# Performance work log

Measured on AMD Instinct MI355X. Metric: run time of the kernel, lower is better.

Reference implementation:

```python
import jax, jax.numpy as jnp
import numpy as np

N_NODES = 100000
N_EDGES = 300000
N_GRAPHS = 128
NODE_VOCAB = 200
NODE_DIM = 128
EDGE_VOCAB = 8
EDGE_DIM = 64
K_LAYERS = 3


def setup_inputs() -> dict:
    key = jax.random.key(0)
    ks = iter(jax.random.split(key, 40))
    f = lambda shape: jax.random.normal(next(ks), shape, dtype=jnp.float32)
    s = lambda shape: f(shape) * 0.05
    inp = {}
    inp["x_s"] = f((N_NODES, NODE_VOCAB))
    inp["x_t"] = f((N_NODES, NODE_VOCAB))
    inp["edge_attr_s"] = f((2 * N_EDGES, EDGE_VOCAB))
    inp["edge_attr_t"] = f((2 * N_EDGES, EDGE_VOCAB))
    inp["edge_index_s"] = jax.random.randint(next(ks), (2, N_EDGES), 0, N_NODES)
    inp["edge_index_t"] = jax.random.randint(next(ks), (2, N_EDGES), 0, N_NODES)
    inp["x_s_batch"] = jnp.sort(jax.random.randint(next(ks), (N_NODES,), 0, N_GRAPHS))
    inp["x_t_batch"] = jnp.sort(jax.random.randint(next(ks), (N_NODES,), 0, N_GRAPHS))
    inp["y"] = jax.random.randint(next(ks), (N_GRAPHS,), 0, 2)
    cat = 2 * NODE_DIM + EDGE_DIM  # 320: [x_src, edge_attr, x_dst]
    inp["node_emb"] = s((NODE_VOCAB, NODE_DIM))
    inp["edge_emb"] = s((EDGE_VOCAB, EDGE_DIM))
    inp["W_in_0"] = s((K_LAYERS, cat, EDGE_DIM))
    inp["W_in_1"] = s((K_LAYERS, EDGE_DIM, 1))
    inp["W_out_0"] = s((K_LAYERS, cat, EDGE_DIM))
    inp["W_out_1"] = s((K_LAYERS, EDGE_DIM, 1))
    inp["Wg_in"] = s((K_LAYERS, NODE_DIM, NODE_DIM))
    inp["bg_in"] = jnp.zeros((K_LAYERS, NODE_DIM), jnp.float32)
    inp["Wg_out"] = s((K_LAYERS, NODE_DIM, NODE_DIM))
    inp["bg_out"] = jnp.zeros((K_LAYERS, NODE_DIM), jnp.float32)
    inp["cls_W0"] = s((2 * NODE_DIM, NODE_DIM))
    inp["cls_b0"] = jnp.zeros((NODE_DIM,), jnp.float32)
    inp["cls_W1"] = s((NODE_DIM, 2))
    inp["cls_b1"] = jnp.zeros((2,), jnp.float32)
    return inp


def _dag_embed(x, e, row, col, W_in_0, W_in_1, W_out_0, W_out_1, Wg_in, bg_in, Wg_out, bg_out):
    N = x.shape[0]
    E = row.shape[0]
    for k in range(W_in_0.shape[0]):
        e_in, e_out = e[:E], e[E:]  # chunk(edge_attr_x, 2, dim=0)
        info_in = jnp.concatenate([x[row], e_in, x[col]], axis=1)   # [E, 2D+Ce]
        info_out = jnp.concatenate([x[col], e_out, x[row]], axis=1)
        e_in = info_in @ W_in_0[k]
        e_out = info_out @ W_out_0[k]
        w_in = jax.nn.sigmoid(e_in @ W_in_1[k]).ravel()   # [E]
        w_out = jax.nn.sigmoid(e_out @ W_out_1[k]).ravel()
        # embedding_in: flow source->target (x_j = x[row], aggregate at col)
        xi = x @ Wg_in[k]
        x_in = jax.ops.segment_sum(w_in[:, None] * xi[row], col, num_segments=N) + bg_in[k]
        # embedding_out: flow target->source (x_j = x[col], aggregate at row)
        xo = x @ Wg_out[k]
        x_out = jax.ops.segment_sum(w_out[:, None] * xo[col], row, num_segments=N) + bg_out[k]
        x = x + x_in + x_out
        e = jnp.concatenate([e_in, e_out], axis=0)
    return x


def _mean_pool(x, batch, num_graphs):
    sums = jax.ops.segment_sum(x, batch, num_segments=num_graphs)
    cnt = jax.ops.segment_sum(jnp.ones((x.shape[0], 1), x.dtype), batch, num_segments=num_graphs)
    return sums / jnp.maximum(cnt, 1.0)


def reference(x_s, x_t, edge_attr_s, edge_attr_t, edge_index_s, edge_index_t,
              x_s_batch, x_t_batch, y, node_emb, edge_emb,
              W_in_0, W_in_1, W_out_0, W_out_1, Wg_in, bg_in, Wg_out, bg_out,
              cls_W0, cls_b0, cls_W1, cls_b1):
    # Initialization: argmax -> embedding lookup
    h_s = node_emb[jnp.argmax(x_s, axis=1)]
    h_t = node_emb[jnp.argmax(x_t, axis=1)]
    he_s = edge_emb[jnp.argmax(edge_attr_s, axis=1)]
    he_t = edge_emb[jnp.argmax(edge_attr_t, axis=1)]
    h_s = _dag_embed(h_s, he_s, edge_index_s[0], edge_index_s[1],
                     W_in_0, W_in_1, W_out_0, W_out_1, Wg_in, bg_in, Wg_out, bg_out)
    h_t = _dag_embed(h_t, he_t, edge_index_t[0], edge_index_t[1],
                     W_in_0, W_in_1, W_out_0, W_out_1, Wg_in, bg_in, Wg_out, bg_out)
    g_s = _mean_pool(h_s, x_s_batch, N_GRAPHS)
    g_t = _mean_pool(h_t, x_t_batch, N_GRAPHS)
    h = jax.nn.relu(jnp.concatenate([g_s, g_t], axis=1) @ cls_W0 + cls_b0)
    logits = h @ cls_W1 + cls_b1
    logp = jax.nn.log_softmax(logits, axis=1)
    loss = -jnp.mean(jnp.take_along_axis(logp, y[:, None], axis=1))
    return loss
```

## Files before the change

### kernel.cpp

```cpp
#include <hip/hip_runtime.h>
#include <hip/hip_bf16.h>

#define N_NODES 100000
#define N_EDGES 300000
#define N_GRAPHS 128
#define NODE_VOCAB 200
#define NODE_DIM 128
#define EDGE_DIM 64
#define K_LAYERS 3

#define SCAN_CHUNK 2048
#define SCAN_NBLK ((N_NODES + SCAN_CHUNK - 1) / SCAN_CHUNK)

typedef unsigned short ushort_t;
typedef __attribute__((ext_vector_type(8))) __bf16 bf16x8;
typedef __attribute__((ext_vector_type(4))) float f32x4;

__device__ inline ushort_t f2bf(float f) {
    unsigned int u = __float_as_uint(f);
    unsigned int r = (u + 0x7fff + ((u >> 16) & 1)) >> 16;
    return (ushort_t)r;
}
__device__ inline float bf2f(ushort_t u) {
    return __uint_as_float(((unsigned int)u) << 16);
}
__device__ inline float bflo(unsigned int u) { return __uint_as_float(u << 16); }
__device__ inline float bfhi(unsigned int u) { return __uint_as_float(u & 0xffff0000u); }

#define MASK_J0 0x15151515u
#define MASK_J1 0x28282828u
#define MASK_J2 0x40404040u

__device__ ushort_t g_hb[2][(size_t)N_NODES * NODE_DIM];
__device__ ushort_t g_XWx_b[(size_t)N_NODES * 256];
__device__ ushort_t g_WcatT[256 * 128];
__device__ ushort_t g_QT[K_LAYERS][32][128];
__device__ float g_scal[(size_t)N_NODES * 32];
__device__ float g_bias[8][6];
__device__ int  g_evoc[2 * N_EDGES];
__device__ float g_gsum[2][N_GRAPHS * NODE_DIM];
__device__ float g_cnt[2][N_GRAPHS];
__device__ float g_H[N_GRAPHS * NODE_DIM];
__device__ int  g_deg_in[N_NODES];
__device__ int  g_deg_out[N_NODES];
__device__ int  g_off_in[N_NODES + 1];
__device__ int  g_off_out[N_NODES + 1];
__device__ int  g_cur_in[N_NODES];
__device__ int  g_cur_out[N_NODES];
__device__ int2 g_lst_in[N_EDGES];
__device__ int2 g_lst_out[N_EDGES];
__device__ int  g_bsum[2][SCAN_NBLK];
__device__ int  g_boff[2][SCAN_NBLK];

__global__ void node_embed_kernel(const float* __restrict__ x, const float* __restrict__ emb,
                                  int N) {
    int wave = threadIdx.x >> 6;
    int lane = threadIdx.x & 63;
    int n = blockIdx.x * 4 + wave;
    if (n >= N) return;
    const float* xr = x + (size_t)n * NODE_VOCAB;
    float v = xr[lane];
    int idx = lane;
    float nv = xr[lane + 64];
    if (nv > v) { v = nv; idx = lane + 64; }
    nv = xr[lane + 128];
    if (nv > v) { v = nv; idx = lane + 128; }
    if (lane < NODE_VOCAB - 192) {
        nv = xr[lane + 192];
        if (nv > v) { v = nv; idx = lane + 192; }
    }
    #pragma unroll
    for (int off = 32; off; off >>= 1) {
        float ov = __shfl_xor(v, off);
        int oi = __shfl_xor(idx, off);
        if (ov > v || (ov == v && oi < idx)) { v = ov; idx = oi; }
    }
    const float* er = emb + (size_t)idx * NODE_DIM;
    g_hb[0][(size_t)n * NODE_DIM + lane] = f2bf(er[lane]);
    g_hb[0][(size_t)n * NODE_DIM + 64 + lane] = f2bf(er[64 + lane]);
}

__global__ void edge_voc_kernel(const float* __restrict__ ea, int M) {
    long idx = (long)blockIdx.x * 256 + threadIdx.x;
    if (idx >= M) return;
    const float* ar = ea + idx * 8;
    float4 v0 = *(const float4*)ar;
    float4 v1 = *(const float4*)(ar + 4);
    float vals[8] = {v0.x, v0.y, v0.z, v0.w, v1.x, v1.y, v1.z, v1.w};
    int best = 0;
    float bv = vals[0];
    #pragma unroll
    for (int i = 1; i < 8; ++i)
        if (vals[i] > bv) { bv = vals[i]; best = i; }
    g_evoc[idx] = best;
}

__global__ void zero_qt_kernel() {
    int i = blockIdx.x * 256 + threadIdx.x;
    if (i < K_LAYERS * 32 * 128) ((ushort_t*)g_QT)[i] = 0;
}

__global__ void setup_gates_kernel(const float* __restrict__ Wi0, const float* __restrict__ Wi1,
                                   const float* __restrict__ Wo0, const float* __restrict__ Wo1,
                                   const float* __restrict__ eemb) {
    int b = blockIdx.x;
    int D = b / 3, k = b % 3;
    int t = threadIdx.x;
    const float* W0 = D ? Wo0 : Wi0;
    const float* W1 = D ? Wo1 : Wi1;
    __shared__ float u[64], un[64];
    if (t < 64) u[t] = W1[k * 64 + t];
    __syncthreads();
    int offk = (k == 0) ? 0 : (k == 1 ? 2 : 4);
    for (int j = k; j >= 0; --j) {
        const float* Wj = W0 + (size_t)j * 320 * 64;
        float qa = 0.f, qc = 0.f;
        for (int m = 0; m < 64; ++m) {
            float um = u[m];
            qa += Wj[t * 64 + m] * um;
            qc += Wj[(192 + t) * 64 + m] * um;
        }
        g_QT[j][(D ? 8 : 0) + offk + j][t] = f2bf(qa);
        g_QT[j][(D ? 24 : 16) + offk + j][t] = f2bf(qc);
        float s = 0.f;
        if (t < 64) {
            for (int m = 0; m < 64; ++m) s += Wj[(128 + t) * 64 + m] * u[m];
        }
        __syncthreads();
        if (t < 64) un[t] = s;
        __syncthreads();
        if (t < 64) u[t] = un[t];
        __syncthreads();
    }
    if (t < 8) {
        float s = 0.f;
        for (int m = 0; m < 64; ++m) s += eemb[t * 64 + m] * u[m];
        g_bias[t][D * 3 + k] = s;
    }
}

__global__ void csr_zero_kernel() {
    int i = blockIdx.x * 256 + threadIdx.x;
    if (i < N_NODES) { g_deg_in[i] = 0; g_deg_out[i] = 0; }
}

__global__ void csr_count_kernel(const int* __restrict__ row, const int* __restrict__ col,
                                 int E) {
    int e = blockIdx.x * 256 + threadIdx.x;
    if (e >= E) return;
    atomicAdd(&g_deg_in[col[e]], 1);
    atomicAdd(&g_deg_out[row[e]], 1);
}

__global__ void csr_bsum_kernel() {
    int which = blockIdx.y;
    const int* deg = which ? g_deg_out : g_deg_in;
    int b = blockIdx.x;
    int t = threadIdx.x;
    int base = b * SCAN_CHUNK;
    int s = 0;
    #pragma unroll
    for (int i = 0; i < SCAN_CHUNK / 256; ++i) {
        int idx = base + i * 256 + t;
        if (idx < N_NODES) s += deg[idx];
    }
    __shared__ int red[256];
    red[t] = s;
    __syncthreads();
    for (int d = 128; d; d >>= 1) {
        if (t < d) red[t] += red[t + d];
        __syncthreads();
    }
    if (t == 0) g_bsum[which][b] = red[0];
}

__global__ void csr_bscan_kernel() {
    int which = blockIdx.x;
    int t = threadIdx.x;
    int v = (t < SCAN_NBLK) ? g_bsum[which][t] : 0;
    int orig = v;
    #pragma unroll
    for (int d = 1; d < 64; d <<= 1) {
        int u = __shfl_up(v, d, 64);
        if (t >= d) v += u;
    }
    if (t < SCAN_NBLK) g_boff[which][t] = v - orig;
}

__global__ void csr_off_kernel(int total) {
    int which = blockIdx.y;
    const int* deg = which ? g_deg_out : g_deg_in;
    int* off = which ? g_off_out : g_off_in;
    int* cur = which ? g_cur_out : g_cur_in;
    int b = blockIdx.x;
    int t = threadIdx.x;
    const int per = SCAN_CHUNK / 256;
    int lo = b * SCAN_CHUNK + t * per;
    int d8[per];
    int s = 0;
    #pragma unroll
    for (int i = 0; i < per; ++i) {
        int idx = lo + i;
        d8[i] = (idx < N_NODES) ? deg[idx] : 0;
        s += d8[i];
    }
    __shared__ int part[256];
    part[t] = s;
    __syncthreads();
    for (int d = 1; d < 256; d <<= 1) {
        int add = (t >= d) ? part[t - d] : 0;
        __syncthreads();
        part[t] += add;
        __syncthreads();
    }
    int run = g_boff[which][b] + part[t] - s;
    #pragma unroll
    for (int i = 0; i < per; ++i) {
        int idx = lo + i;
        if (idx < N_NODES) {
            off[idx] = run;
            cur[idx] = run;
            run += d8[i];
        }
    }
    if (b == 0 && t == 0) off[N_NODES] = total;
}

__global__ void csr_fill_kernel(const int* __restrict__ row, const int* __restrict__ col,
                                int E) {
    int e = blockIdx.x * 256 + threadIdx.x;
    if (e >= E) return;
    int r = row[e], c = col[e];
    int p = atomicAdd(&g_cur_in[c], 1);
    g_lst_in[p] = make_int2(r, g_evoc[e]);
    int q = atomicAdd(&g_cur_out[r], 1);
    g_lst_out[q] = make_int2(c, g_evoc[E + e]);
}

__global__ void assemble_wcat(const float* __restrict__ Wgi, const float* __restrict__ Wgo) {
    int idx = blockIdx.x * 256 + threadIdx.x;
    int n = idx >> 7;
    int kd = idx & 127;
    float v = (n < 128) ? Wgi[kd * 128 + n] : Wgo[kd * 128 + (n - 128)];
    g_WcatT[n * 128 + kd] = f2bf(v);
}

__global__ __launch_bounds__(320) void gemm_xw_mfma(int cur, int layer, unsigned int mask,
                                                    int M) {
    const ushort_t* __restrict__ hb = g_hb[cur];
    int m0 = blockIdx.x * 64;
    int t = threadIdx.x;
    int wave = t >> 6, lane = t & 63;
    __shared__ ushort_t As[64 * 128];

    for (int idx = t; idx < 1024; idx += 320) {
        int m = idx >> 4, c = idx & 15;
        int gm = m0 + m;
        uint4 v = make_uint4(0u, 0u, 0u, 0u);
        if (gm < M) v = *(const uint4*)(hb + (size_t)gm * 128 + c * 8);
        *(uint4*)&As[m * 128 + ((c * 8) ^ ((m & 7) << 3))] = v;
    }
    __syncthreads();

    int lr = lane & 15, lk = lane >> 4;

    if (wave < 4) {
        int nbase = wave * 64;
        f32x4 acc[4][4];
        #pragma unroll
        for (int i = 0; i < 4; ++i)
            #pragma unroll
            for (int j = 0; j < 4; ++j)
                acc[i][j] = (f32x4){0.f, 0.f, 0.f, 0.f};

        const ushort_t* Bbase = g_WcatT + (size_t)nbase * 128;
        #pragma unroll
        for (int ks = 0; ks < 4; ++ks) {
            bf16x8 a[4], b[4];
            int ke = ks * 32 + lk * 8;
            #pragma unroll
            for (int mt = 0; mt < 4; ++mt) {
                int row = mt * 16 + lr;
                a[mt] = *(const bf16x8*)&As[row * 128 + (ke ^ ((row & 7) << 3))];
            }
            #pragma unroll
            for (int nt = 0; nt < 4; ++nt) {
                b[nt] = *(const bf16x8*)(Bbase + (size_t)(nt * 16 + lr) * 128 + ke);
            }
            #pragma unroll
            for (int mt = 0; mt < 4; ++mt)
                #pragma unroll
                for (int nt = 0; nt < 4; ++nt)
                    acc[mt][nt] = __builtin_amdgcn_mfma_f32_16x16x32_bf16(a[mt], b[nt], acc[mt][nt], 0, 0, 0);
        }

        #pragma unroll
        for (int mt = 0; mt < 4; ++mt) {
            #pragma unroll
            for (int r = 0; r < 4; ++r) {
                int gm = m0 + mt * 16 + lk * 4 + r;
                if (gm >= M) continue;
                #pragma unroll
                for (int nt = 0; nt < 4; ++nt) {
                    int n = nbase + nt * 16 + lr;
                    g_XWx_b[(size_t)gm * 256 + n] = f2bf(acc[mt][nt][r]);
                }
            }
        }
    } else {
        const ushort_t* QT = &g_QT[layer][0][0];
        f32x4 acc[4][2];
        #pragma unroll
        for (int i = 0; i < 4; ++i)
            #pragma unroll
            for (int j = 0; j < 2; ++j)
                acc[i][j] = (f32x4){0.f, 0.f, 0.f, 0.f};

        #pragma unroll
        for (int ks = 0; ks < 4; ++ks) {
            bf16x8 a[4], b[2];
            int ke = ks * 32 + lk * 8;
            #pragma unroll
            for (int mt = 0; mt < 4; ++mt) {
                int row = mt * 16 + lr;
                a[mt] = *(const bf16x8*)&As[row * 128 + (ke ^ ((row & 7) << 3))];
            }
            #pragma unroll
            for (int nt = 0; nt < 2; ++nt)
                b[nt] = *(const bf16x8*)&QT[(nt * 16 + lr) * 128 + ke];
            #pragma unroll
            for (int mt = 0; mt < 4; ++mt)
                #pragma unroll
                for (int nt = 0; nt < 2; ++nt)
                    acc[mt][nt] = __builtin_amdgcn_mfma_f32_16x16x32_bf16(a[mt], b[nt], acc[mt][nt], 0, 0, 0);
        }

        #pragma unroll
        for (int mt = 0; mt < 4; ++mt)
            #pragma unroll
            for (int r = 0; r < 4; ++r) {
                int gm = m0 + mt * 16 + lk * 4 + r;
                if (gm >= M) continue;
                #pragma unroll
                for (int nt = 0; nt < 2; ++nt) {
                    int colc = nt * 16 + lr;
                    if ((mask >> colc) & 1u)
                        g_scal[(size_t)gm * 32 + colc] = acc[mt][nt][r];
                }
            }
    }
}

__global__ __launch_bounds__(256) void aggregate_kernel(int cur, int k,
                                                        const float* __restrict__ bgi,
                                                        const float* __restrict__ bgo, int N) {
    int wv = threadIdx.x >> 6;
    int lane = threadIdx.x & 63;
    int grp = lane >> 4, li = lane & 15;
    int n = blockIdx.x * 4 + wv;
    if (n >= N) return;
    float bias_in = g_bias[lane & 7][k];
    float bias_out = g_bias[lane & 7][3 + k];
    const float* srow = g_scal + (size_t)n * 32;
    float cin, cout;
    if (k == 0) {
        cin = srow[16]; cout = srow[24];
    } else if (k == 1) {
        float2 a = *(const float2*)(srow + 18);
        float2 b = *(const float2*)(srow + 26);
        cin = a.x + a.y; cout = b.x + b.y;
    } else {
        float4 a = *(const float4*)(srow + 20);
        float4 b = *(const float4*)(srow + 28);
        cin = a.x + a.y + a.z; cout = b.x + b.y + b.z;
    }
    float acc[8];
    if (grp == 0) {
        uint4 xv = *(const uint4*)(g_hb[cur] + (size_t)n * 128 + li * 8);
        float4 b1 = *(const float4*)(bgi + li * 8);
        float4 b2 = *(const float4*)(bgi + li * 8 + 4);
        float4 c1 = *(const float4*)(bgo + li * 8);
        float4 c2 = *(const float4*)(bgo + li * 8 + 4);
        acc[0] = bflo(xv.x) + b1.x + c1.x;
        acc[1] = bfhi(xv.x) + b1.y + c1.y;
        acc[2] = bflo(xv.y) + b1.z + c1.z;
        acc[3] = bfhi(xv.y) + b1.w + c1.w;
        acc[4] = bflo(xv.z) + b2.x + c2.x;
        acc[5] = bfhi(xv.z) + b2.y + c2.y;
        acc[6] = bflo(xv.w) + b2.z + c2.z;
        acc[7] = bfhi(xv.w) + b2.w + c2.w;
    } else {
        #pragma unroll
        for (int q = 0; q < 8; ++q) acc[q] = 0.f;
    }
    int p0 = g_off_in[n], p1 = g_off_in[n + 1];
    for (int p = p0 + grp; p < p1; p += 4) {
        int2 se = g_lst_in[p];
        const float* arow = g_scal + (size_t)se.x * 32;
        float asum;
        if (k == 0) asum = arow[0];
        else if (k == 1) { float2 t2 = *(const float2*)(arow + 2); asum = t2.x + t2.y; }
        else { float4 t4 = *(const float4*)(arow + 4); asum = t4.x + t4.y + t4.z; }
        float s = __shfl(bias_in, se.y) + asum + cin;
        float wvv = 1.0f / (1.0f + __expf(-s));
        uint4 pv = *(const uint4*)(g_XWx_b + (size_t)se.x * 256 + li * 8);
        acc[0] += wvv * bflo(pv.x);
        acc[1] += wvv * bfhi(pv.x);
        acc[2] += wvv * bflo(pv.y);
        acc[3] += wvv * bfhi(pv.y);
        acc[4] += wvv * bflo(pv.z);
        acc[5] += wvv * bfhi(pv.z);
        acc[6] += wvv * bflo(pv.w);
        acc[7] += wvv * bfhi(pv.w);
    }
    p0 = g_off_out[n]; p1 = g_off_out[n + 1];
    for (int p = p0 + grp; p < p1; p += 4) {
        int2 se = g_lst_out[p];
        const float* arow = g_scal + (size_t)se.x * 32;
        float asum;
        if (k == 0) asum = arow[8];
        else if (k == 1) { float2 t2 = *(const float2*)(arow + 10); asum = t2.x + t2.y; }
        else { float4 t4 = *(const float4*)(arow + 12); asum = t4.x + t4.y + t4.z; }
        float s = __shfl(bias_out, se.y) + asum + cout;
        float wvv = 1.0f / (1.0f + __expf(-s));
        uint4 pv = *(const uint4*)(g_XWx_b + (size_t)se.x * 256 + 128 + li * 8);
        acc[0] += wvv * bflo(pv.x);
        acc[1] += wvv * bfhi(pv.x);
        acc[2] += wvv * bflo(pv.y);
        acc[3] += wvv * bfhi(pv.y);
        acc[4] += wvv * bflo(pv.z);
        acc[5] += wvv * bfhi(pv.z);
        acc[6] += wvv * bflo(pv.w);
        acc[7] += wvv * bfhi(pv.w);
    }
    #pragma unroll
    for (int q = 0; q < 8; ++q) {
        acc[q] += __shfl_xor(acc[q], 16);
        acc[q] += __shfl_xor(acc[q], 32);
    }
    if (grp == 0) {
        uint4 pk;
        pk.x = ((unsigned int)f2bf(acc[1]) << 16) | (unsigned int)f2bf(acc[0]);
        pk.y = ((unsigned int)f2bf(acc[3]) << 16) | (unsigned int)f2bf(acc[2]);
        pk.z = ((unsigned int)f2bf(acc[5]) << 16) | (unsigned int)f2bf(acc[4]);
        pk.w = ((unsigned int)f2bf(acc[7]) << 16) | (unsigned int)f2bf(acc[6]);
        *(uint4*)(g_hb[cur ^ 1] + (size_t)n * 128 + li * 8) = pk;
    }
}

__global__ void pool_kernel(int fin, int side, const int* __restrict__ batch, int N) {
    const ushort_t* x = g_hb[fin];
    float* gsum = g_gsum[side];
    int n0 = blockIdx.x * 128;
    int d = threadIdx.x;
    if (n0 >= N) return;
    int nend = min(n0 + 128, N);
    float acc = 0.f;
    int curg = batch[n0];
    for (int n = n0; n < nend; ++n) {
        int g = batch[n];
        if (g != curg) {
            atomicAdd(&gsum[curg * 128 + d], acc);
            acc = 0.f;
            curg = g;
        }
        acc += bf2f(x[(size_t)n * 128 + d]);
    }
    atomicAdd(&gsum[curg * 128 + d], acc);
}

__global__ void count_kernel(int side, const int* __restrict__ batch, int N) {
    int g = threadIdx.x;
    int lo = 0, hi = N;
    while (lo < hi) { int mid = (lo + hi) >> 1; if (batch[mid] < g) lo = mid + 1; else hi = mid; }
    int a = lo;
    lo = 0; hi = N;
    while (lo < hi) { int mid = (lo + hi) >> 1; if (batch[mid] < g + 1) lo = mid + 1; else hi = mid; }
    g_cnt[side][g] = (float)(lo - a);
}

__global__ void zero_gsum_kernel() {
    int i = blockIdx.x * 256 + threadIdx.x;
    if (i < 2 * N_GRAPHS * NODE_DIM) ((float*)g_gsum)[i] = 0.f;
}

__global__ void hidden_kernel(const float* __restrict__ W0, const float* __restrict__ b0) {
    int g = blockIdx.x;
    int j = threadIdx.x;
    float inv_s = 1.0f / fmaxf(g_cnt[0][g], 1.0f);
    float inv_t = 1.0f / fmaxf(g_cnt[1][g], 1.0f);
    float acc = b0[j];
    for (int k = 0; k < 128; ++k) acc += g_gsum[0][g * 128 + k] * inv_s * W0[k * 128 + j];
    for (int k = 0; k < 128; ++k) acc += g_gsum[1][g * 128 + k] * inv_t * W0[(128 + k) * 128 + j];
    g_H[g * 128 + j] = fmaxf(acc, 0.f);
}

__global__ void loss_kernel(const float* __restrict__ W1, const float* __restrict__ b1,
                            const int* __restrict__ y, float* __restrict__ out) {
    int g = threadIdx.x;
    float l0 = b1[0], l1 = b1[1];
    for (int j = 0; j < 128; ++j) {
        float hv = g_H[g * 128 + j];
        l0 += hv * W1[j * 2 + 0];
        l1 += hv * W1[j * 2 + 1];
    }
    float m = fmaxf(l0, l1);
    float lse = m + logf(expf(l0 - m) + expf(l1 - m));
    float ly = (y[g] == 0) ? l0 : l1;
    float c = -(ly - lse) * (1.0f / (float)N_GRAPHS);
    __shared__ float red[128];
    red[g] = c;
    __syncthreads();
    for (int s = 64; s; s >>= 1) {
        if (g < s) red[g] += red[g + s];
        __syncthreads();
    }
    if (g == 0) out[0] = red[0];
}

extern "C" void kernel_launch(void* const* d_in, const int* in_sizes, int n_in,
                              void* d_out, int out_size, void* d_ws, size_t ws_size,
                              hipStream_t stream) {
    const float* x_s      = (const float*)d_in[0];
    const float* x_t      = (const float*)d_in[1];
    const float* ea_s     = (const float*)d_in[2];
    const float* ea_t     = (const float*)d_in[3];
    const int*   ei_s     = (const int*)d_in[4];
    const int*   ei_t     = (const int*)d_in[5];
    const int*   batch_s  = (const int*)d_in[6];
    const int*   batch_t  = (const int*)d_in[7];
    const int*   y        = (const int*)d_in[8];
    const float* node_emb = (const float*)d_in[9];
    const float* edge_emb = (const float*)d_in[10];
    const float* W_in_0   = (const float*)d_in[11];
    const float* W_in_1   = (const float*)d_in[12];
    const float* W_out_0  = (const float*)d_in[13];
    const float* W_out_1  = (const float*)d_in[14];
    const float* Wg_in    = (const float*)d_in[15];
    const float* bg_in    = (const float*)d_in[16];
    const float* Wg_out   = (const float*)d_in[17];
    const float* bg_out   = (const float*)d_in[18];
    const float* cls_W0   = (const float*)d_in[19];
    const float* cls_b0   = (const float*)d_in[20];
    const float* cls_W1   = (const float*)d_in[21];
    const float* cls_b1   = (const float*)d_in[22];

    const int N = N_NODES, E = N_EDGES;
    static const unsigned int MASKS[3] = {MASK_J0, MASK_J1, MASK_J2};

    zero_gsum_kernel<<<(2 * N_GRAPHS * NODE_DIM + 255) / 256, 256, 0, stream>>>();
    zero_qt_kernel<<<(K_LAYERS * 32 * 128 + 255) / 256, 256, 0, stream>>>();
    setup_gates_kernel<<<6, 128, 0, stream>>>(W_in_0, W_in_1, W_out_0, W_out_1, edge_emb);

    for (int side = 0; side < 2; ++side) {
        const float* xin   = side ? x_t : x_s;
        const float* eain  = side ? ea_t : ea_s;
        const int*   ei    = side ? ei_t : ei_s;
        const int*   batch = side ? batch_t : batch_s;
        const int* row = ei;
        const int* col = ei + E;

        node_embed_kernel<<<(N + 3) / 4, 256, 0, stream>>>(xin, node_emb, N);
        edge_voc_kernel<<<(2 * E + 255) / 256, 256, 0, stream>>>(eain, 2 * E);

        csr_zero_kernel<<<(N + 255) / 256, 256, 0, stream>>>();
        csr_count_kernel<<<(E + 255) / 256, 256, 0, stream>>>(row, col, E);
        csr_bsum_kernel<<<dim3(SCAN_NBLK, 2), 256, 0, stream>>>();
        csr_bscan_kernel<<<2, 64, 0, stream>>>();
        csr_off_kernel<<<dim3(SCAN_NBLK, 2), 256, 0, stream>>>(E);
        csr_fill_kernel<<<(E + 255) / 256, 256, 0, stream>>>(row, col, E);

        int cur = 0;
        for (int k = 0; k < K_LAYERS; ++k) {
            assemble_wcat<<<128, 256, 0, stream>>>(Wg_in + (size_t)k * 128 * 128,
                                                   Wg_out + (size_t)k * 128 * 128);
            gemm_xw_mfma<<<(N + 63) / 64, 320, 0, stream>>>(cur, k, MASKS[k], N);
            aggregate_kernel<<<(N + 3) / 4, 256, 0, stream>>>(
                cur, k, bg_in + (size_t)k * 128, bg_out + (size_t)k * 128, N);
            cur ^= 1;
        }
        pool_kernel<<<(N + 127) / 128, 128, 0, stream>>>(cur, side, batch, N);
        count_kernel<<<1, 128, 0, stream>>>(side, batch, N);
    }

    hidden_kernel<<<128, 128, 0, stream>>>(cls_W0, cls_b0);
    loss_kernel<<<1, 128, 0, stream>>>(cls_W1, cls_b1, y, (float*)d_out);
}
```

Measured before the change: 973.3 us.

## Swap MFMA operands for vectorized stores and batch edge weights in aggregation

New measurement: 922.4 us. 5.2% less time.

```diff
diff --git a/kernel.cpp b/kernel.cpp
--- a/kernel.cpp
+++ b/kernel.cpp
@@ -288,32 +288,33 @@
                 b[nt] = *(const bf16x8*)(Bbase + (size_t)(nt * 16 + lr) * 128 + ke);
             }
             #pragma unroll
-            for (int mt = 0; mt < 4; ++mt)
+            for (int nt = 0; nt < 4; ++nt)
                 #pragma unroll
-                for (int nt = 0; nt < 4; ++nt)
-                    acc[mt][nt] = __builtin_amdgcn_mfma_f32_16x16x32_bf16(a[mt], b[nt], acc[mt][nt], 0, 0, 0);
+                for (int mt = 0; mt < 4; ++mt)
+                    acc[nt][mt] = __builtin_amdgcn_mfma_f32_16x16x32_bf16(b[nt], a[mt], acc[nt][mt], 0, 0, 0);
         }
 
         #pragma unroll
         for (int mt = 0; mt < 4; ++mt) {
-            #pragma unroll
-            for (int r = 0; r < 4; ++r) {
-                int gm = m0 + mt * 16 + lk * 4 + r;
-                if (gm >= M) continue;
-                #pragma unroll
-                for (int nt = 0; nt < 4; ++nt) {
-                    int n = nbase + nt * 16 + lr;
-                    g_XWx_b[(size_t)gm * 256 + n] = f2bf(acc[mt][nt][r]);
-                }
+            int gm = m0 + mt * 16 + lr;
+            if (gm >= M) continue;
+            #pragma unroll
+            for (int nt = 0; nt < 4; ++nt) {
+                int n0 = nbase + nt * 16 + lk * 4;
+                f32x4 av = acc[nt][mt];
+                uint2 pk;
+                pk.x = ((unsigned int)f2bf(av[1]) << 16) | (unsigned int)f2bf(av[0]);
+                pk.y = ((unsigned int)f2bf(av[3]) << 16) | (unsigned int)f2bf(av[2]);
+                *(uint2*)&g_XWx_b[(size_t)gm * 256 + n0] = pk;
             }
         }
     } else {
         const ushort_t* QT = &g_QT[layer][0][0];
-        f32x4 acc[4][2];
-        #pragma unroll
-        for (int i = 0; i < 4; ++i)
-            #pragma unroll
-            for (int j = 0; j < 2; ++j)
+        f32x4 acc[2][4];
+        #pragma unroll
+        for (int i = 0; i < 2; ++i)
+            #pragma unroll
+            for (int j = 0; j < 4; ++j)
                 acc[i][j] = (f32x4){0.f, 0.f, 0.f, 0.f};
 
         #pragma unroll
@@ -329,31 +330,34 @@
             for (int nt = 0; nt < 2; ++nt)
                 b[nt] = *(const bf16x8*)&QT[(nt * 16 + lr) * 128 + ke];
             #pragma unroll
-            for (int mt = 0; mt < 4; ++mt)
+            for (int nt = 0; nt < 2; ++nt)
                 #pragma unroll
-                for (int nt = 0; nt < 2; ++nt)
-                    acc[mt][nt] = __builtin_amdgcn_mfma_f32_16x16x32_bf16(a[mt], b[nt], acc[mt][nt], 0, 0, 0);
-        }
-
-        #pragma unroll
-        for (int mt = 0; mt < 4; ++mt)
-            #pragma unroll
-            for (int r = 0; r < 4; ++r) {
-                int gm = m0 + mt * 16 + lk * 4 + r;
-                if (gm >= M) continue;
+                for (int mt = 0; mt < 4; ++mt)
+                    acc[nt][mt] = __builtin_amdgcn_mfma_f32_16x16x32_bf16(b[nt], a[mt], acc[nt][mt], 0, 0, 0);
+        }
+
+        #pragma unroll
+        for (int mt = 0; mt < 4; ++mt) {
+            int gm = m0 + mt * 16 + lr;
+            if (gm >= M) continue;
+            #pragma unroll
+            for (int nt = 0; nt < 2; ++nt) {
                 #pragma unroll
-                for (int nt = 0; nt < 2; ++nt) {
-                    int colc = nt * 16 + lr;
+                for (int r = 0; r < 4; ++r) {
+                    int colc = nt * 16 + lk * 4 + r;
                     if ((mask >> colc) & 1u)
-                        g_scal[(size_t)gm * 32 + colc] = acc[mt][nt][r];
+                        g_scal[(size_t)gm * 32 + colc] = acc[nt][mt][r];
                 }
             }
+        }
     }
 }
 
 __global__ __launch_bounds__(256) void aggregate_kernel(int cur, int k,
                                                         const float* __restrict__ bgi,
                                                         const float* __restrict__ bgo, int N) {
+    __shared__ float sW[4][64];
+    __shared__ int sS[4][64];
     int wv = threadIdx.x >> 6;
     int lane = threadIdx.x & 63;
     int grp = lane >> 4, li = lane & 15;
@@ -366,14 +370,15 @@
     if (k == 0) {
         cin = srow[16]; cout = srow[24];
     } else if (k == 1) {
-        float2 a = *(const float2*)(srow + 18);
-        float2 b = *(const float2*)(srow + 26);
-        cin = a.x + a.y; cout = b.x + b.y;
+        cin = srow[18] + srow[19]; cout = srow[26] + srow[27];
     } else {
-        float4 a = *(const float4*)(srow + 20);
-        float4 b = *(const float4*)(srow + 28);
-        cin = a.x + a.y + a.z; cout = b.x + b.y + b.z;
-    }
+        cin = srow[20] + srow[21] + srow[22];
+        cout = srow[28] + srow[29] + srow[30];
+    }
+    int pin0 = g_off_in[n], din = g_off_in[n + 1] - pin0;
+    int pout0 = g_off_out[n], dout = g_off_out[n + 1] - pout0;
+    int tot = din + dout;
+
     float acc[8];
     if (grp == 0) {
         uint4 xv = *(const uint4*)(g_hb[cur] + (size_t)n * 128 + li * 8);
@@ -393,45 +398,40 @@
         #pragma unroll
         for (int q = 0; q < 8; ++q) acc[q] = 0.f;
     }
-    int p0 = g_off_in[n], p1 = g_off_in[n + 1];
-    for (int p = p0 + grp; p < p1; p += 4) {
-        int2 se = g_lst_in[p];
-        const float* arow = g_scal + (size_t)se.x * 32;
-        float asum;
-        if (k == 0) asum = arow[0];
-        else if (k == 1) { float2 t2 = *(const float2*)(arow + 2); asum = t2.x + t2.y; }
-        else { float4 t4 = *(const float4*)(arow + 4); asum = t4.x + t4.y + t4.z; }
-        float s = __shfl(bias_in, se.y) + asum + cin;
-        float wvv = 1.0f / (1.0f + __expf(-s));
-        uint4 pv = *(const uint4*)(g_XWx_b + (size_t)se.x * 256 + li * 8);
-        acc[0] += wvv * bflo(pv.x);
-        acc[1] += wvv * bfhi(pv.x);
-        acc[2] += wvv * bflo(pv.y);
-        acc[3] += wvv * bfhi(pv.y);
-        acc[4] += wvv * bflo(pv.z);
-        acc[5] += wvv * bfhi(pv.z);
-        acc[6] += wvv * bflo(pv.w);
-        acc[7] += wvv * bfhi(pv.w);
-    }
-    p0 = g_off_out[n]; p1 = g_off_out[n + 1];
-    for (int p = p0 + grp; p < p1; p += 4) {
-        int2 se = g_lst_out[p];
-        const float* arow = g_scal + (size_t)se.x * 32;
-        float asum;
-        if (k == 0) asum = arow[8];
-        else if (k == 1) { float2 t2 = *(const float2*)(arow + 10); asum = t2.x + t2.y; }
-        else { float4 t4 = *(const float4*)(arow + 12); asum = t4.x + t4.y + t4.z; }
-        float s = __shfl(bias_out, se.y) + asum + cout;
-        float wvv = 1.0f / (1.0f + __expf(-s));
-        uint4 pv = *(const uint4*)(g_XWx_b + (size_t)se.x * 256 + 128 + li * 8);
-        acc[0] += wvv * bflo(pv.x);
-        acc[1] += wvv * bfhi(pv.x);
-        acc[2] += wvv * bflo(pv.y);
-        acc[3] += wvv * bfhi(pv.y);
-        acc[4] += wvv * bflo(pv.z);
-        acc[5] += wvv * bfhi(pv.z);
-        acc[6] += wvv * bflo(pv.w);
-        acc[7] += wvv * bfhi(pv.w);
+
+    for (int base = 0; base < tot; base += 64) {
+        int cnt = min(64, tot - base);
+        if (lane < cnt) {
+            int q = base + lane;
+            int2 se;
+            int dir;
+            if (q < din) { se = g_lst_in[pin0 + q]; dir = 0; }
+            else         { se = g_lst_out[pout0 + q - din]; dir = 1; }
+            const float* arow = g_scal + (size_t)se.x * 32 + dir * 8;
+            float asum;
+            if (k == 0) asum = arow[0];
+            else if (k == 1) asum = arow[2] + arow[3];
+            else asum = arow[4] + arow[5] + arow[6];
+            float bi = __shfl(bias_in, se.y);
+            float bo = __shfl(bias_out, se.y);
+            float s = (dir ? bo : bi) + asum + (dir ? cout : cin);
+            sW[wv][lane] = 1.0f / (1.0f + __expf(-s));
+            sS[wv][lane] = se.x * 2 + dir;
+        }
+        for (int e = grp; e < cnt; e += 4) {
+            float wvv = sW[wv][e];
+            int sv = sS[wv][e];
+            const ushort_t* src = g_XWx_b + (size_t)(sv >> 1) * 256 + (sv & 1) * 128 + li * 8;
+            uint4 pv = *(const uint4*)src;
+            acc[0] += wvv * bflo(pv.x);
+            acc[1] += wvv * bfhi(pv.x);
+            acc[2] += wvv * bflo(pv.y);
+            acc[3] += wvv * bfhi(pv.y);
+            acc[4] += wvv * bflo(pv.z);
+            acc[5] += wvv * bfhi(pv.z);
+            acc[6] += wvv * bflo(pv.w);
+            acc[7] += wvv * bfhi(pv.w);
+        }
     }
     #pragma unroll
     for (int q = 0; q < 8; ++q) {
```
